# Kernel tuning notes

Hardware: AMD Instinct MI355X
Metric: run time of the kernel (lower is better)

Reference implementation:

```python
import jax, jax.numpy as jnp
import numpy as np

D_MODEL = 1024
NUM_HEADS = 16

def _dense_params(key, d_in, d_out):
    kw, _ = jax.random.split(key)
    # flax default: lecun_normal kernel, zeros bias
    W = jax.random.normal(kw, (d_in, d_out), dtype=jnp.float32) / np.sqrt(d_in)
    b = jnp.zeros((d_out,), dtype=jnp.float32)
    return W, b

def setup_inputs() -> dict:
    key = jax.random.key(0)
    ks = jax.random.split(key, 8)
    B, Tx, Tc = 2, 2048, 2048
    x = jax.random.normal(ks[0], (B, Tx, D_MODEL), dtype=jnp.float32)
    context = jax.random.normal(ks[1], (B, Tc, D_MODEL), dtype=jnp.float32)
    Wq, bq = _dense_params(ks[2], D_MODEL, D_MODEL)
    Wks, bks = _dense_params(ks[3], D_MODEL, D_MODEL)
    Wvs, bvs = _dense_params(ks[4], D_MODEL, D_MODEL)
    Wkc, bkc = _dense_params(ks[5], D_MODEL, D_MODEL)
    Wvc, bvc = _dense_params(ks[6], D_MODEL, D_MODEL)
    Wo, bo = _dense_params(ks[7], D_MODEL, D_MODEL)
    return {"x": x, "context": context,
            "Wq": Wq, "bq": bq, "Wks": Wks, "bks": bks, "Wvs": Wvs, "bvs": bvs,
            "Wkc": Wkc, "bkc": bkc, "Wvc": Wvc, "bvc": bvc, "Wo": Wo, "bo": bo}

def _split_heads(t, H):
    B, T, C = t.shape
    return t.reshape(B, T, H, C // H).transpose(0, 2, 1, 3)  # [B,H,T,hd]

def reference(x, context, Wq, bq, Wks, bks, Wvs, bvs, Wkc, bkc, Wvc, bvc, Wo, bo):
    H = NUM_HEADS
    head_dim = D_MODEL // H
    q = x @ Wq + bq
    k = jnp.concatenate([x @ Wks + bks, context @ Wkc + bkc], axis=1)
    v = jnp.concatenate([x @ Wvs + bvs, context @ Wvc + bvc], axis=1)
    q = _split_heads(q, H)  # [B,H,Tq,hd]
    k = _split_heads(k, H)  # [B,H,Tk,hd]
    v = _split_heads(v, H)
    attn = jnp.einsum('bhqd,bhkd->bhqk', q, k) / jnp.sqrt(jnp.float32(head_dim))
    attn = jax.nn.softmax(attn, axis=-1)
    out = jnp.einsum('bhqk,bhkd->bhqd', attn, v)
    B, _, Tq, _ = out.shape
    out = out.transpose(0, 2, 1, 3).reshape(B, Tq, D_MODEL)
    return out @ Wo + bo
```

## Files before the change

### kernel.cpp

```cpp
#include <hip/hip_runtime.h>
#include <hip/hip_bf16.h>
#include <math.h>


typedef _Float16 f16;
typedef _Float16 f16x8 __attribute__((ext_vector_type(8)));
typedef _Float16 f16x4v __attribute__((ext_vector_type(4)));
typedef float    f32x4 __attribute__((ext_vector_type(4)));

#define MFMA_F16(a, b, c) __builtin_amdgcn_mfma_f32_16x16x32_f16((a), (b), (c), 0, 0, 0)

#define QSCALE 0.18033688011112042f

__device__ __forceinline__ void glds16(const f16* g, f16* l) {
    __builtin_amdgcn_global_load_lds(
        (const __attribute__((address_space(1))) void*)g,
        (__attribute__((address_space(3))) void*)l, 16, 0, 0);
}

__global__ __launch_bounds__(256) void prep(
    const float4* __restrict__ x, const float4* __restrict__ ctx,
    f16x4v* __restrict__ xb, f16x4v* __restrict__ cb,
    const float* __restrict__ W0, const float* __restrict__ W1,
    const float* __restrict__ W2, const float* __restrict__ W3,
    const float* __restrict__ W4, const float* __restrict__ W5,
    f16* __restrict__ wt)
{
    if (blockIdx.x < 8192) {
        const int n4 = (2 * 2048 * 1024) / 4;
        int i = blockIdx.x * 256 + threadIdx.x;
        float4 v;
        f16x4v* dst;
        if (i < n4) { v = x[i];        dst = xb + i; }
        else        { v = ctx[i - n4]; dst = cb + (i - n4); }
        f16x4v h = { (f16)v.x, (f16)v.y, (f16)v.z, (f16)v.w };
        *dst = h;
        return;
    }
    const int idx = blockIdx.x - 8192;
    const int z = idx >> 10, rem = idx & 1023;
    const float* Ws[6] = { W0, W1, W2, W3, W4, W5 };
    const float* W = Ws[z];
    f16* Wt = wt + (size_t)z * (1024 * 1024);

    __shared__ float tile[32][33];
    const int tx = threadIdx.x & 31, ty = threadIdx.x >> 5;
    const int n0 = (rem & 31) * 32, k0 = (rem >> 5) * 32;

#pragma unroll
    for (int i = 0; i < 4; ++i) {
        int r = i * 8 + ty;
        tile[r][tx] = W[(size_t)(k0 + r) * 1024 + n0 + tx];
    }
    __syncthreads();
#pragma unroll
    for (int i = 0; i < 4; ++i) {
        int r = i * 8 + ty;
        Wt[(size_t)(n0 + r) * 1024 + k0 + tx] = (f16)tile[tx][r];
    }
}

#define GEMM_PROLOGUE(BN)                                                     \
    const int m0 = blockIdx.x * 128, n0 = blockIdx.y * (BN);                  \
    const int tid = threadIdx.x;                                              \
    const int w = tid >> 6, lane = tid & 63, quad = lane >> 4, l15 = lane & 15;\
    const int wm = (w >> 1) * 64, wn = (w & 1) * ((BN) / 2);                  \
    const int qsw = (quad ^ ((l15 >> 1) & 3)) * 8;                            \
    int gA[2], gB[(BN) / 64];                                                 \
    _Pragma("unroll")                                                         \
    for (int p = 0; p < 2; ++p) {                                             \
        int s = tid + p * 256;                                                \
        int r = (s >> 2) & 127, c = (s & 3) ^ ((s >> 3) & 3);                 \
        gA[p] = (m0 + r) * 1024 + c * 8;                                      \
    }                                                                         \
    _Pragma("unroll")                                                         \
    for (int p = 0; p < (BN) / 64; ++p) {                                     \
        int s = tid + p * 256;                                                \
        int r = (s >> 2) & ((BN) - 1), c = (s & 3) ^ ((s >> 3) & 3);          \
        gB[p] = (n0 + r) * 1024 + c * 8;                                      \
    }

#define GEMM_STAGE_TO(BN, buf, koff)                                          \
    _Pragma("unroll")                                                         \
    for (int p = 0; p < 2; ++p)                                               \
        glds16(&A[gA[p] + (koff)], &As[buf][(p * 256 + w * 64) * 8]);         \
    _Pragma("unroll")                                                         \
    for (int p = 0; p < (BN) / 64; ++p)                                       \
        glds16(&Bt[gB[p] + (koff)], &Bs[buf][(p * 256 + w * 64) * 8]);

__global__ __launch_bounds__(256) void proj_gemm(
    const f16* __restrict__ xb, const f16* __restrict__ cb,
    const f16* __restrict__ wt,
    const float* __restrict__ bq, const float* __restrict__ bks,
    const float* __restrict__ bkc, const float* __restrict__ bvs,
    const float* __restrict__ bvc,
    f16* __restrict__ qbuf, f16* __restrict__ kbuf, f16* __restrict__ vbuf)
{
    __shared__ alignas(16) f16 As[2][128 * 32];
    __shared__ alignas(16) f16 Bs[2][128 * 32];

    const int z = blockIdx.z;
    const f16* A = (z == 0 || z == 1 || z == 3) ? xb : cb;
    const int wslot = (z == 0) ? 0 : (z == 1) ? 1 : (z == 2) ? 3 : (z == 3) ? 2 : 4;
    const f16* Bt = wt + (size_t)wslot * 1048576;
    const float* bias = (z == 0) ? bq : (z == 1) ? bks : (z == 2) ? bkc
                        : (z == 3) ? bvs : bvc;
    const int roff = (z == 2 || z == 4) ? 2048 : 0;

    GEMM_PROLOGUE(128)
    f32x4 acc[4][4] = {};

    GEMM_STAGE_TO(128, 0, 0)

    for (int k0 = 0; k0 < 1024; k0 += 32) {
        const int cur = (k0 >> 5) & 1;
        __syncthreads();
        if (k0 + 32 < 1024) {
            GEMM_STAGE_TO(128, cur ^ 1, k0 + 32)
        }
        f16x8 a[4], b[4];
#pragma unroll
        for (int i = 0; i < 4; ++i)
            a[i] = *(const f16x8*)&As[cur][(wm + i * 16 + l15) * 32 + qsw];
#pragma unroll
        for (int i = 0; i < 4; ++i)
            b[i] = *(const f16x8*)&Bs[cur][(wn + i * 16 + l15) * 32 + qsw];
#pragma unroll
        for (int mi = 0; mi < 4; ++mi)
#pragma unroll
            for (int ni = 0; ni < 4; ++ni)
                acc[mi][ni] = MFMA_F16(a[mi], b[ni], acc[mi][ni]);
    }

#pragma unroll
    for (int mi = 0; mi < 4; ++mi) {
#pragma unroll
        for (int r = 0; r < 4; ++r) {
            int row = m0 + wm + mi * 16 + quad * 4 + r;
            int b_ = row >> 11, tok = row & 2047;
#pragma unroll
            for (int ni = 0; ni < 4; ++ni) {
                int col = n0 + wn + ni * 16 + l15;
                float v = acc[mi][ni][r] + bias[col];
                int bh = b_ * 16 + (col >> 6);
                int tg = roff + tok;
                if (z == 0) {
                    qbuf[((size_t)bh * 2048 + tok) * 64 + (col & 63)] = (f16)(v * QSCALE);
                } else if (z <= 2) {
                    kbuf[(size_t)bh * 262144 + (size_t)(tg >> 6) * 4096
                         + (size_t)((col >> 5) & 1) * 2048 + (tg & 63) * 32 + (col & 31)] = (f16)v;
                } else {
                    vbuf[(size_t)bh * 262144 + (size_t)tg * 64 + (col & 63)] = (f16)v;
                }
            }
        }
    }
}

__global__ __launch_bounds__(256) void transpose_v(
    const f16* __restrict__ vbuf, f16* __restrict__ vt)
{
    const int t = threadIdx.x;
    const int mt = t >> 3, md = t & 7;
    const int tok0 = blockIdx.x * 256 + mt * 8;
    const int z = blockIdx.y;
    f16x8 in[8];
#pragma unroll
    for (int i = 0; i < 8; ++i)
        in[i] = *(const f16x8*)&vbuf[((size_t)z * 4096 + tok0 + i) * 64 + md * 8];
    f16x8 ov[8];
#pragma unroll
    for (int j = 0; j < 8; ++j)
#pragma unroll
        for (int i = 0; i < 8; ++i) ov[j][i] = in[i][j];
    const int kt = tok0 >> 6, kks = (tok0 >> 5) & 1, kko = tok0 & 31;
#pragma unroll
    for (int j = 0; j < 8; ++j)
        *(f16x8*)&vt[(size_t)z * 262144 + (size_t)kt * 4096 + kks * 2048
                     + (md * 8 + j) * 32 + kko] = ov[j];
}

__global__ __launch_bounds__(256, 2) void attn_kernel(
    const f16* __restrict__ q, const f16* __restrict__ kb,
    const f16* __restrict__ vtb, f16* __restrict__ osplit,
    float* __restrict__ lsplit)
{
    __shared__ alignas(16) f16 K_lds[2][4096];
    __shared__ alignas(16) f16 V_lds[2][4096];
    __shared__ alignas(16) f16 P_lds[128 * 72];

    const int tid = threadIdx.x;
    const int w = tid >> 6, lane = tid & 63, quad = lane >> 4, l15 = lane & 15;
    const int bh = blockIdx.x, qt = blockIdx.y, sp = blockIdx.z;
    const int qbase = qt * 128;

    f16x8 qa[2][2];
#pragma unroll
    for (int nq = 0; nq < 2; ++nq) {
        const size_t qaddr =
            ((size_t)bh * 2048 + qbase + w * 32 + nq * 16 + l15) * 64 + quad * 8;
        qa[nq][0] = *(const f16x8*)&q[qaddr];
        qa[nq][1] = *(const f16x8*)&q[qaddr + 32];
    }

    f16x8 ones;
#pragma unroll
    for (int j = 0; j < 8; ++j) ones[j] = (f16)1.0f;

    f32x4 o_acc[2][4] = {};
    f32x4 l_acc[2] = {};

    const f16* ktile = kb + (size_t)bh * 262144 + (size_t)sp * 131072;
    const f16* vtile = vtb + (size_t)bh * 262144 + (size_t)sp * 131072;

    const int sco = ((tid >> 2) * 4 + ((tid & 3) ^ ((tid >> 3) & 3))) * 8;
    const int qsw = (quad ^ ((l15 >> 1) & 3)) * 8;
    const int wslot = w * 512;

    glds16(ktile + sco,        &K_lds[0][wslot]);
    glds16(ktile + 2048 + sco, &K_lds[0][2048 + wslot]);
    glds16(vtile + sco,        &V_lds[0][wslot]);
    glds16(vtile + 2048 + sco, &V_lds[0][2048 + wslot]);

    for (int kt = 0; kt < 32; ++kt) {
        const f16* Kc = K_lds[kt & 1];
        const f16* Vc = V_lds[kt & 1];
        f16* Kn = K_lds[(kt + 1) & 1];
        f16* Vn = V_lds[(kt + 1) & 1];

        __syncthreads();

        ktile += 4096; vtile += 4096;
        glds16(ktile + sco,        Kn + wslot);
        glds16(ktile + 2048 + sco, Kn + 2048 + wslot);
        glds16(vtile + sco,        Vn + wslot);
        glds16(vtile + 2048 + sco, Vn + 2048 + wslot);

        f32x4 s[4][2];
        __builtin_amdgcn_s_setprio(1);
#pragma unroll
        for (int mt = 0; mt < 4; ++mt) {
            f16x8 ka0 = *(const f16x8*)&Kc[(mt * 16 + l15) * 32 + qsw];
            f16x8 ka1 = *(const f16x8*)&Kc[2048 + (mt * 16 + l15) * 32 + qsw];
#pragma unroll
            for (int nq = 0; nq < 2; ++nq) {
                f32x4 t = {};
                t = MFMA_F16(ka0, qa[nq][0], t);
                t = MFMA_F16(ka1, qa[nq][1], t);
                s[mt][nq] = t;
            }
        }
        __builtin_amdgcn_s_setprio(0);

#pragma unroll
        for (int mt = 0; mt < 4; ++mt) {
#pragma unroll
            for (int nq = 0; nq < 2; ++nq) {
                f16x4v pk;
#pragma unroll
                for (int r = 0; r < 4; ++r)
                    pk[r] = (f16)__builtin_amdgcn_exp2f(s[mt][nq][r]);
                *(f16x4v*)&P_lds[(w * 32 + nq * 16 + l15) * 72 + mt * 16 + quad * 4] = pk;
            }
        }

        f16x8 pa[2][2];
#pragma unroll
        for (int nq = 0; nq < 2; ++nq)
#pragma unroll
            for (int ks = 0; ks < 2; ++ks)
                pa[nq][ks] = *(const f16x8*)&P_lds[(w * 32 + nq * 16 + l15) * 72 + ks * 32 + quad * 8];

        __builtin_amdgcn_s_setprio(1);
#pragma unroll
        for (int nq = 0; nq < 2; ++nq) {
            l_acc[nq] = MFMA_F16(ones, pa[nq][0], l_acc[nq]);
            l_acc[nq] = MFMA_F16(ones, pa[nq][1], l_acc[nq]);
        }

#pragma unroll
        for (int dt = 0; dt < 4; ++dt) {
            f16x8 vb0 = *(const f16x8*)&Vc[(dt * 16 + l15) * 32 + qsw];
            f16x8 vb1 = *(const f16x8*)&Vc[2048 + (dt * 16 + l15) * 32 + qsw];
#pragma unroll
            for (int nq = 0; nq < 2; ++nq) {
                o_acc[nq][dt] = MFMA_F16(pa[nq][0], vb0, o_acc[nq][dt]);
                o_acc[nq][dt] = MFMA_F16(pa[nq][1], vb1, o_acc[nq][dt]);
            }
        }
        __builtin_amdgcn_s_setprio(0);
    }

    const size_t sb = (size_t)(sp * 32 + bh) * 2048 + qbase;
#pragma unroll
    for (int nq = 0; nq < 2; ++nq) {
        if (quad == 0)
            lsplit[sb + w * 32 + nq * 16 + l15] = l_acc[nq][0];
#pragma unroll
        for (int r = 0; r < 4; ++r) {
            float lr = __shfl(l_acc[nq][0], quad * 4 + r, 64);
            float inv = 1.0f / lr;
            int ql = w * 32 + nq * 16 + quad * 4 + r;
            size_t obase = (sb + ql) * 64;
#pragma unroll
            for (int dt = 0; dt < 4; ++dt)
                osplit[obase + dt * 16 + l15] = (f16)(o_acc[nq][dt][r] * inv);
        }
    }
}

__global__ __launch_bounds__(256) void combine(
    const f16* __restrict__ osplit, const float* __restrict__ lsplit,
    f16* __restrict__ abuf)
{
    int idx = blockIdx.x * 256 + threadIdx.x;
    int d8 = idx & 7;
    int row = (idx >> 3) & 2047;
    int bh = idx >> 14;
    int b = bh >> 4, h = bh & 15;
    size_t base1 = ((size_t)bh * 2048 + row) * 64 + d8 * 8;
    size_t base2 = ((size_t)(32 + bh) * 2048 + row) * 64 + d8 * 8;
    float l1 = lsplit[bh * 2048 + row];
    float l2 = lsplit[(32 + bh) * 2048 + row];
    float inv = 1.0f / (l1 + l2);
    float w1 = l1 * inv, w2 = l2 * inv;
    f16x8 a = *(const f16x8*)&osplit[base1];
    f16x8 c = *(const f16x8*)&osplit[base2];
    f16x8 out;
#pragma unroll
    for (int j = 0; j < 8; ++j)
        out[j] = (f16)(w1 * (float)a[j] + w2 * (float)c[j]);
    *(f16x8*)&abuf[((size_t)(b * 2048 + row)) * 1024 + h * 64 + d8 * 8] = out;
}

__global__ __launch_bounds__(256) void out_gemm(
    const f16* __restrict__ abuf, const f16* __restrict__ wt5,
    const float* __restrict__ bo, float* __restrict__ out)
{
    __shared__ alignas(16) f16 As[2][128 * 32];
    __shared__ alignas(16) f16 Bs[2][64 * 32];

    const f16* A = abuf;
    const f16* Bt = wt5;

    GEMM_PROLOGUE(64)
    f32x4 acc[4][2] = {};

    GEMM_STAGE_TO(64, 0, 0)

    for (int k0 = 0; k0 < 1024; k0 += 32) {
        const int cur = (k0 >> 5) & 1;
        __syncthreads();
        if (k0 + 32 < 1024) {
            GEMM_STAGE_TO(64, cur ^ 1, k0 + 32)
        }
        f16x8 a[4], b[2];
#pragma unroll
        for (int i = 0; i < 4; ++i)
            a[i] = *(const f16x8*)&As[cur][(wm + i * 16 + l15) * 32 + qsw];
#pragma unroll
        for (int i = 0; i < 2; ++i)
            b[i] = *(const f16x8*)&Bs[cur][(wn + i * 16 + l15) * 32 + qsw];
#pragma unroll
        for (int mi = 0; mi < 4; ++mi)
#pragma unroll
            for (int ni = 0; ni < 2; ++ni)
                acc[mi][ni] = MFMA_F16(a[mi], b[ni], acc[mi][ni]);
    }

#pragma unroll
    for (int mi = 0; mi < 4; ++mi) {
#pragma unroll
        for (int r = 0; r < 4; ++r) {
            int row = m0 + wm + mi * 16 + quad * 4 + r;
#pragma unroll
            for (int ni = 0; ni < 2; ++ni) {
                int col = n0 + wn + ni * 16 + l15;
                out[(size_t)row * 1024 + col] = acc[mi][ni][r] + bo[col];
            }
        }
    }
}

extern "C" void kernel_launch(void* const* d_in, const int* in_sizes, int n_in,
                              void* d_out, int out_size, void* d_ws, size_t ws_size,
                              hipStream_t stream)
{
    (void)in_sizes; (void)n_in; (void)out_size; (void)ws_size;

    const float* x    = (const float*)d_in[0];
    const float* ctx  = (const float*)d_in[1];
    const float* Wq   = (const float*)d_in[2];  const float* bq  = (const float*)d_in[3];
    const float* Wks  = (const float*)d_in[4];  const float* bks = (const float*)d_in[5];
    const float* Wvs  = (const float*)d_in[6];  const float* bvs = (const float*)d_in[7];
    const float* Wkc  = (const float*)d_in[8];  const float* bkc = (const float*)d_in[9];
    const float* Wvc  = (const float*)d_in[10]; const float* bvc = (const float*)d_in[11];
    const float* Wo   = (const float*)d_in[12]; const float* bo  = (const float*)d_in[13];

    char* ws = (char*)d_ws;
    f16*   xb     = (f16*)(ws + 0);
    f16*   cb     = (f16*)(ws + 8388608);
    f16*   vt     = (f16*)(ws + 0);
    f16*   wt     = (f16*)(ws + 16777216);
    float* lsplit = (float*)(ws + 16777216);
    f16*   qbuf   = (f16*)(ws + 29360128);
    f16*   kbuf   = (f16*)(ws + 37748736);
    f16*   vbuf   = (f16*)(ws + 54525952);
    f16*   osplit = (f16*)(ws + 54525952);
    f16*   abuf   = (f16*)(ws + 71303168);

    prep<<<14336, 256, 0, stream>>>((const float4*)x, (const float4*)ctx,
                                    (f16x4v*)xb, (f16x4v*)cb,
                                    Wq, Wks, Wvs, Wkc, Wvc, Wo, wt);

    proj_gemm<<<dim3(32, 8, 5), 256, 0, stream>>>(
        xb, cb, wt, bq, bks, bkc, bvs, bvc, qbuf, kbuf, vbuf);

    transpose_v<<<dim3(16, 32), 256, 0, stream>>>(vbuf, vt);

    attn_kernel<<<dim3(32, 16, 2), 256, 0, stream>>>(qbuf, kbuf, vt, osplit, lsplit);

    combine<<<2048, 256, 0, stream>>>(osplit, lsplit, abuf);

    out_gemm<<<dim3(32, 16), 256, 0, stream>>>(abuf, wt + 5 * 1048576, bo, (float*)d_out);
}
```

Before: 306.9 us.

## Single-buffer K/V LDS with register prefetch to raise attention occupancy

Replaces the double-buffered K/V LDS tiles, filled by direct global-to-LDS loads, with single buffers. The next tile is prefetched into registers during compute and written to LDS after an extra barrier. This halves K/V LDS use so launch bounds can ask for 4 blocks per CU instead of 2. The QK^T and exp stages are also interleaved per row tile to cut live score registers. The cost is a second __syncthreads per iteration, more register pressure from the prefetch, and possible spills under the tighter register limit.

```diff
diff --git a/kernel.cpp b/kernel.cpp
--- a/kernel.cpp
+++ b/kernel.cpp
@@ -180,13 +180,13 @@
                      + (md * 8 + j) * 32 + kko] = ov[j];
 }
 
-__global__ __launch_bounds__(256, 2) void attn_kernel(
+__global__ __launch_bounds__(256, 4) void attn_kernel(
     const f16* __restrict__ q, const f16* __restrict__ kb,
     const f16* __restrict__ vtb, f16* __restrict__ osplit,
     float* __restrict__ lsplit)
 {
-    __shared__ alignas(16) f16 K_lds[2][4096];
-    __shared__ alignas(16) f16 V_lds[2][4096];
+    __shared__ alignas(16) f16 K_lds[4096];
+    __shared__ alignas(16) f16 V_lds[4096];
     __shared__ alignas(16) f16 P_lds[128 * 72];
 
     const int tid = threadIdx.x;
@@ -216,50 +216,45 @@
     const int sco = ((tid >> 2) * 4 + ((tid & 3) ^ ((tid >> 3) & 3))) * 8;
     const int qsw = (quad ^ ((l15 >> 1) & 3)) * 8;
     const int wslot = w * 512;
-
-    glds16(ktile + sco,        &K_lds[0][wslot]);
-    glds16(ktile + 2048 + sco, &K_lds[0][2048 + wslot]);
-    glds16(vtile + sco,        &V_lds[0][wslot]);
-    glds16(vtile + 2048 + sco, &V_lds[0][2048 + wslot]);
+    const int lslot = wslot + lane * 8;
+
+    glds16(ktile + sco,        &K_lds[wslot]);
+    glds16(ktile + 2048 + sco, &K_lds[2048 + wslot]);
+    glds16(vtile + sco,        &V_lds[wslot]);
+    glds16(vtile + 2048 + sco, &V_lds[2048 + wslot]);
 
     for (int kt = 0; kt < 32; ++kt) {
-        const f16* Kc = K_lds[kt & 1];
-        const f16* Vc = V_lds[kt & 1];
-        f16* Kn = K_lds[(kt + 1) & 1];
-        f16* Vn = V_lds[(kt + 1) & 1];
-
         __syncthreads();
 
         ktile += 4096; vtile += 4096;
-        glds16(ktile + sco,        Kn + wslot);
-        glds16(ktile + 2048 + sco, Kn + 2048 + wslot);
-        glds16(vtile + sco,        Vn + wslot);
-        glds16(vtile + 2048 + sco, Vn + 2048 + wslot);
-
-        f32x4 s[4][2];
-        __builtin_amdgcn_s_setprio(1);
+        f16x8 kn0, kn1, vn0, vn1;
+        if (kt != 31) {
+            kn0 = *(const f16x8*)&ktile[sco];
+            kn1 = *(const f16x8*)&ktile[2048 + sco];
+            vn0 = *(const f16x8*)&vtile[sco];
+            vn1 = *(const f16x8*)&vtile[2048 + sco];
+        }
+
 #pragma unroll
         for (int mt = 0; mt < 4; ++mt) {
-            f16x8 ka0 = *(const f16x8*)&Kc[(mt * 16 + l15) * 32 + qsw];
-            f16x8 ka1 = *(const f16x8*)&Kc[2048 + (mt * 16 + l15) * 32 + qsw];
+            f16x8 ka0 = *(const f16x8*)&K_lds[(mt * 16 + l15) * 32 + qsw];
+            f16x8 ka1 = *(const f16x8*)&K_lds[2048 + (mt * 16 + l15) * 32 + qsw];
+            f32x4 s[2];
+            __builtin_amdgcn_s_setprio(1);
 #pragma unroll
             for (int nq = 0; nq < 2; ++nq) {
                 f32x4 t = {};
                 t = MFMA_F16(ka0, qa[nq][0], t);
                 t = MFMA_F16(ka1, qa[nq][1], t);
-                s[mt][nq] = t;
+                s[nq] = t;
             }
-        }
-        __builtin_amdgcn_s_setprio(0);
-
-#pragma unroll
-        for (int mt = 0; mt < 4; ++mt) {
+            __builtin_amdgcn_s_setprio(0);
 #pragma unroll
             for (int nq = 0; nq < 2; ++nq) {
                 f16x4v pk;
 #pragma unroll
                 for (int r = 0; r < 4; ++r)
-                    pk[r] = (f16)__builtin_amdgcn_exp2f(s[mt][nq][r]);
+                    pk[r] = (f16)__builtin_amdgcn_exp2f(s[nq][r]);
                 *(f16x4v*)&P_lds[(w * 32 + nq * 16 + l15) * 72 + mt * 16 + quad * 4] = pk;
             }
         }
@@ -280,8 +275,8 @@
 
 #pragma unroll
         for (int dt = 0; dt < 4; ++dt) {
-            f16x8 vb0 = *(const f16x8*)&Vc[(dt * 16 + l15) * 32 + qsw];
-            f16x8 vb1 = *(const f16x8*)&Vc[2048 + (dt * 16 + l15) * 32 + qsw];
+            f16x8 vb0 = *(const f16x8*)&V_lds[(dt * 16 + l15) * 32 + qsw];
+            f16x8 vb1 = *(const f16x8*)&V_lds[2048 + (dt * 16 + l15) * 32 + qsw];
 #pragma unroll
             for (int nq = 0; nq < 2; ++nq) {
                 o_acc[nq][dt] = MFMA_F16(pa[nq][0], vb0, o_acc[nq][dt]);
@@ -289,6 +284,14 @@
             }
         }
         __builtin_amdgcn_s_setprio(0);
+
+        __syncthreads();
+        if (kt != 31) {
+            *(f16x8*)&K_lds[lslot]        = kn0;
+            *(f16x8*)&K_lds[2048 + lslot] = kn1;
+            *(f16x8*)&V_lds[lslot]        = vn0;
+            *(f16x8*)&V_lds[2048 + lslot] = vn1;
+        }
     }
 
     const size_t sb = (size_t)(sp * 32 + bh) * 2048 + qbase;
```

Result: faster. 300.0 us (-2.3%).
